# Kernel optimization log

Hardware: AMD Instinct MI355X
Metric: run time of the kernel (lower is better)

## Reference

```python
import jax, jax.numpy as jnp
import numpy as np

N_NODES = 50000
N_EDGES = 800000
N_REL = 16
D = 64          # entity_dim == relation_dim == n_hidden
NEG_SLOPE = 0.01  # torch F.leaky_relu default


def setup_inputs() -> dict:
    key = jax.random.key(0)
    ks = jax.random.split(key, 12)
    s = 1.0 / np.sqrt(D)
    return {
        "node_ids": jnp.arange(N_NODES, dtype=jnp.int64) if jax.config.jax_enable_x64 else jnp.arange(N_NODES, dtype=jnp.int32),
        "relation_ids": jax.random.randint(ks[0], (N_EDGES,), 0, N_REL),
        "src": jax.random.randint(ks[1], (N_EDGES,), 0, N_NODES),
        "dst": jax.random.randint(ks[2], (N_EDGES,), 0, N_NODES),
        "entity_embed": jax.random.normal(ks[3], (N_NODES, D), jnp.float32) * s,
        "relation_embed": jax.random.normal(ks[4], (N_REL, D), jnp.float32) * s,
        "W0": jax.random.normal(ks[5], (N_REL, D, D), jnp.float32) * s,
        "W1": jax.random.normal(ks[6], (N_REL, D, D), jnp.float32) * s,
        "ra0": jax.random.normal(ks[7], (D, D), jnp.float32) * s,
        "rb0": jax.random.normal(ks[8], (D, D), jnp.float32) * s,
        "ra1": jax.random.normal(ks[9], (D, D), jnp.float32) * s,
        "rb1": jax.random.normal(ks[10], (D, D), jnp.float32) * s,
    }


def _edge_softmax(scores, dst, n_nodes):
    # segment softmax over edges grouped by destination node (DGL edge_softmax)
    m = jax.ops.segment_max(scores, dst, num_segments=n_nodes)  # [N]
    e = jnp.exp(scores - m[dst])                                # [E]
    z = jax.ops.segment_sum(e, dst, num_segments=n_nodes)       # [N]
    return e / z[dst]


def _kgat_layer(h, efeat, src, dst, etype, Wr, ra, rb, n_nodes):
    # transform every node under every relation once: [N, R, Dr]
    trans = jnp.einsum('nd,rde->nre', h, Wr)
    t_r = trans[src, etype]                   # W_r h_t  [E, Dr]
    h_r = trans[dst, etype]                   # W_r h_h  [E, Dr]
    att = jnp.sum(t_r * jnp.tanh(h_r + efeat), axis=1)  # [E]
    a = _edge_softmax(att, dst, n_nodes)                 # [E]
    # u_mul_e + sum: scatter-add weighted source features to dst
    h_nb = jax.ops.segment_sum(h[src] * a[:, None], dst, num_segments=n_nodes)
    # Bi residual
    out = (jax.nn.leaky_relu((h + h_nb) @ ra, NEG_SLOPE)
           + jax.nn.leaky_relu((h * h_nb) @ rb, NEG_SLOPE))
    return out


def reference(node_ids, relation_ids, src, dst, entity_embed, relation_embed,
              W0, W1, ra0, rb0, ra1, rb1):
    h = entity_embed[node_ids]                 # [N, D]
    efeat = relation_embed[relation_ids]       # [E, D]
    n_nodes = node_ids.shape[0]
    cache = [h]
    for Wr, ra, rb in ((W0, ra0, rb0), (W1, ra1, rb1)):
        h = _kgat_layer(h, efeat, src, dst, relation_ids, Wr, ra, rb, n_nodes)
        cache.append(h)
    return jnp.concatenate(cache, axis=1)      # [N, 3*D]
```

## Files before the change

### kernel.cpp

```cpp
#include <hip/hip_runtime.h>
#include <hip/hip_bf16.h>
#include <math.h>

#define NN 50000
#define NE 800000
#define NR 16
#define DD 64
#define OSTRIDE 192
#define QSTRIDE 1032

typedef _Float16 f16;
typedef f16 f16x8 __attribute__((ext_vector_type(8)));
typedef f16 f16x2 __attribute__((ext_vector_type(2)));
typedef __attribute__((ext_vector_type(4))) float f32x4;

__device__ inline float tanh_fast(float x) {
    return 1.f - 2.f / (__expf(2.f * x) + 1.f);
}

__device__ inline float dot2acc(f16x2 a, f16x2 b, float c) {
#if __has_builtin(__builtin_amdgcn_fdot2)
    return __builtin_amdgcn_fdot2(a, b, c, false);
#else
    return c + (float)a[0] * (float)b[0] + (float)a[1] * (float)b[1];
#endif
}

#if __has_builtin(__builtin_amdgcn_update_dpp)
__device__ inline float xor1_add(float x) {
    return x + __int_as_float(__builtin_amdgcn_update_dpp(
        0, __float_as_int(x), 0xB1, 0xF, 0xF, true));
}
__device__ inline float xor2_add(float x) {
    return x + __int_as_float(__builtin_amdgcn_update_dpp(
        0, __float_as_int(x), 0x4E, 0xF, 0xF, true));
}
__device__ inline float xor8_add(float x) {
    return x + __int_as_float(__builtin_amdgcn_update_dpp(
        0, __float_as_int(x), 0x108, 0xF, 0xF, true));
}
#else
__device__ inline float xor1_add(float x) { return x + __shfl_xor(x, 1, 64); }
__device__ inline float xor2_add(float x) { return x + __shfl_xor(x, 2, 64); }
__device__ inline float xor8_add(float x) { return x + __shfl_xor(x, 8, 64); }
#endif

__global__ void k_deg(const int* __restrict__ dst, int* __restrict__ cnt) {
    for (int e = blockIdx.x * blockDim.x + threadIdx.x; e < NE;
         e += gridDim.x * blockDim.x)
        atomicAdd(&cnt[dst[e]], 1);
}

__global__ __launch_bounds__(256) void k_scan1(const int* __restrict__ cnt,
                                               int* __restrict__ rowptr,
                                               int* __restrict__ bsum) {
    __shared__ int sh[256];
    int b = blockIdx.x, t = threadIdx.x;
    int i = b * 256 + t;
    int v = (i < NN) ? cnt[i] : 0;
    sh[t] = v;
    __syncthreads();
    #pragma unroll
    for (int o = 1; o < 256; o <<= 1) {
        int u = (t >= o) ? sh[t - o] : 0;
        __syncthreads();
        sh[t] += u;
        __syncthreads();
    }
    if (i < NN) rowptr[i] = sh[t] - v;
    if (t == 255) bsum[b] = sh[255];
}

__global__ __launch_bounds__(256) void k_scan2(int* __restrict__ bsum, int nb) {
    __shared__ int sh[256];
    int t = threadIdx.x;
    int v = (t < nb) ? bsum[t] : 0;
    sh[t] = v;
    __syncthreads();
    #pragma unroll
    for (int o = 1; o < 256; o <<= 1) {
        int u = (t >= o) ? sh[t - o] : 0;
        __syncthreads();
        sh[t] += u;
        __syncthreads();
    }
    if (t < nb) bsum[t] = sh[t] - v;
}

__global__ __launch_bounds__(256) void k_scan3(int* __restrict__ rowptr,
                                               const int* __restrict__ bsum,
                                               int* __restrict__ cursor) {
    int b = blockIdx.x, t = threadIdx.x;
    int i = b * 256 + t;
    if (i < NN) {
        int v = rowptr[i] + bsum[b];
        rowptr[i] = v;
        cursor[i] = v;
    }
    if (i == 0) rowptr[NN] = NE;
}

__global__ void k_fill(const int* __restrict__ dst, const int* __restrict__ src,
                       const int* __restrict__ rel, int* __restrict__ cursor,
                       int* __restrict__ epack) {
    for (int e = blockIdx.x * blockDim.x + threadIdx.x; e < NE;
         e += gridDim.x * blockDim.x) {
        int pos = atomicAdd(&cursor[dst[e]], 1);
        epack[pos] = src[e] | (rel[e] << 16);
    }
}

__global__ void k_copy_h0(const int* __restrict__ node_ids,
                          const float* __restrict__ ent,
                          float* __restrict__ out,
                          f16* __restrict__ hf) {
    int i = blockIdx.x * blockDim.x + threadIdx.x;
    if (i >= NN * DD) return;
    int n = i >> 6, d = i & 63;
    float v = ent[(size_t)node_ids[n] * DD + d];
    out[(size_t)n * OSTRIDE + d] = v;
    hf[(size_t)n * DD + d] = (f16)v;
}

__global__ void k_prep(const float* __restrict__ W,
                       const float* __restrict__ ra, const float* __restrict__ rb,
                       f16* __restrict__ wf, f16* __restrict__ wtf,
                       f16* __restrict__ rat, f16* __restrict__ rbt) {
    int i = blockIdx.x * blockDim.x + threadIdx.x;
    if (i < NR * DD * DD) {
        int r = i >> 12, rem = i & 4095, d = rem >> 6, E = rem & 63;
        f16 v = (f16)W[i];
        wf[i] = v;
        wtf[(r << 12) | (E << 6) | d] = v;
    }
    if (i < DD * DD) {
        int d = i >> 6, dp = i & 63;
        rat[dp * 64 + d] = (f16)ra[i];
        rbt[dp * 64 + d] = (f16)rb[i];
    }
}

__global__ __launch_bounds__(1024) void k_fused10(const f16* __restrict__ hfin,
                                                  const f16* __restrict__ wf,
                                                  const f16* __restrict__ wtf,
                                                  const f16* __restrict__ rat,
                                                  const f16* __restrict__ rbt,
                                                  const float* __restrict__ relE,
                                                  const int* __restrict__ rowptr,
                                                  const int* __restrict__ epack,
                                                  float* __restrict__ out,
                                                  int off_in, int off_out,
                                                  f16* __restrict__ hfout) {
    __shared__ __align__(16) f16 q_lds[16 * QSTRIDE];
    __shared__ __align__(16) f16 u_lds[16][16][72];
    int n0 = blockIdx.x * 16;
    int t  = threadIdx.x;
    int w  = t >> 6, l = t & 63;
    int l15 = l & 15, lg = l >> 4;
    int r = w;

    {
        int ar = n0 + l15;
        const f16* ap = hfin + (size_t)ar * DD + lg * 8;
        f16x8 a0 = *(const f16x8*)ap;
        f16x8 a1 = *(const f16x8*)(ap + 32);

        f32x4 acc[4];
        #pragma unroll
        for (int nt = 0; nt < 4; ++nt) acc[nt] = (f32x4){0.f, 0.f, 0.f, 0.f};
        const f16* wtr = wtf + (r << 12);
        #pragma unroll
        for (int nt = 0; nt < 4; ++nt) {
            const f16* bp = wtr + (nt * 16 + l15) * DD + lg * 8;
            f16x8 b0 = *(const f16x8*)bp;
            f16x8 b1 = *(const f16x8*)(bp + 32);
            acc[nt] = __builtin_amdgcn_mfma_f32_16x16x32_f16(a0, b0, acc[nt], 0, 0, 0);
            acc[nt] = __builtin_amdgcn_mfma_f32_16x16x32_f16(a1, b1, acc[nt], 0, 0, 0);
        }

        #pragma unroll
        for (int nt = 0; nt < 4; ++nt) {
            int E = nt * 16 + l15;
            float er = relE[r * DD + E];
            #pragma unroll
            for (int reg = 0; reg < 4; ++reg)
                u_lds[w][lg * 4 + reg][E] = (f16)tanh_fast(acc[nt][reg] + er);
        }
        asm volatile("s_waitcnt lgkmcnt(0)" ::: "memory");

        const f16* up = &u_lds[w][l15][lg * 8];
        f16x8 u0 = *(const f16x8*)up;
        f16x8 u1 = *(const f16x8*)(up + 32);

        f32x4 q4[4];
        #pragma unroll
        for (int nt = 0; nt < 4; ++nt) q4[nt] = (f32x4){0.f, 0.f, 0.f, 0.f};
        const f16* wr = wf + (r << 12);
        #pragma unroll
        for (int nt = 0; nt < 4; ++nt) {
            const f16* bp = wr + (nt * 16 + l15) * DD + lg * 8;
            f16x8 b0 = *(const f16x8*)bp;
            f16x8 b1 = *(const f16x8*)(bp + 32);
            q4[nt] = __builtin_amdgcn_mfma_f32_16x16x32_f16(u0, b0, q4[nt], 0, 0, 0);
            q4[nt] = __builtin_amdgcn_mfma_f32_16x16x32_f16(u1, b1, q4[nt], 0, 0, 0);
        }

        #pragma unroll
        for (int reg = 0; reg < 4; ++reg) {
            f16* qp = q_lds + (lg * 4 + reg) * QSTRIDE + r * 64 + l15;
            #pragma unroll
            for (int nt = 0; nt < 4; ++nt)
                qp[nt * 16] = (f16)q4[nt][reg];
        }
    }
    __syncthreads();

    int n = n0 + w;
    const f16* ql = q_lds + w * QSTRIDE;
    int row0 = rowptr[n], row1 = rowptr[n + 1];
    int deg = row1 - row0;
    int g  = l >> 3;
    int d8 = l & 7;

    float zr = 0.f;
    float a[8] = {};

    int steps = (deg + 7) >> 3;
    const f16* hb = hfin + (d8 << 3);
    for (int k = 0; k < steps; ++k) {
        int idx = row0 + (k << 3) + g;
        bool ok = idx < row1;
        int p = epack[ok ? idx : row0];
        f16x8 hv = *(const f16x8*)(hb + ((size_t)(p & 0xffff) << 6));
        int rr = p >> 16;
        f16x8 qv = *(const f16x8*)(ql + (rr << 6) + (d8 << 3));
        float dp = 0.f;
        #pragma unroll
        for (int j = 0; j < 4; ++j) {
            f16x2 ha = {hv[2 * j], hv[2 * j + 1]};
            f16x2 qa = {qv[2 * j], qv[2 * j + 1]};
            dp = dot2acc(ha, qa, dp);
        }
        dp = xor1_add(dp);
        dp = xor2_add(dp);
        dp += __shfl_xor(dp, 4, 64);
        float wg = ok ? __expf(dp) : 0.f;
        zr += wg;
        #pragma unroll
        for (int j = 0; j < 8; ++j)
            a[j] = fmaf(wg, (float)hv[j], a[j]);
    }

    zr = xor8_add(zr);
    #pragma unroll
    for (int j = 0; j < 8; ++j) a[j] = xor8_add(a[j]);
    #pragma unroll
    for (int o = 16; o < 64; o <<= 1) {
        zr += __shfl_xor(zr, o, 64);
        #pragma unroll
        for (int j = 0; j < 8; ++j)
            a[j] += __shfl_xor(a[j], o, 64);
    }

    if (g == 0) {
        float inv = (deg > 0) ? 1.f / zr : 0.f;
        f16x8 hrow = *(const f16x8*)(hfin + ((size_t)n << 6) + (d8 << 3));
        f16x8 v1v, v2v;
        #pragma unroll
        for (int j = 0; j < 8; ++j) {
            float h = (float)hrow[j];
            float nb = a[j] * inv;
            v1v[j] = (f16)(h + nb);
            v2v[j] = (f16)(h * nb);
        }
        *(f16x8*)(q_lds + w * QSTRIDE + (d8 << 3)) = v1v;
        *(f16x8*)(q_lds + w * QSTRIDE + 256 + (d8 << 3)) = v2v;
    }
    __syncthreads();

    if (w < 4) {
        const f16* v1p = q_lds + (size_t)l15 * QSTRIDE + lg * 8;
        f16x8 a10 = *(const f16x8*)v1p;
        f16x8 a11 = *(const f16x8*)(v1p + 32);
        const f16* v2p = v1p + 256;
        f16x8 a20 = *(const f16x8*)v2p;
        f16x8 a21 = *(const f16x8*)(v2p + 32);

        const f16* bra = rat + (w * 16 + l15) * 64 + lg * 8;
        f16x8 b10 = *(const f16x8*)bra;
        f16x8 b11 = *(const f16x8*)(bra + 32);
        const f16* brb = rbt + (w * 16 + l15) * 64 + lg * 8;
        f16x8 b20 = *(const f16x8*)brb;
        f16x8 b21 = *(const f16x8*)(brb + 32);

        f32x4 o1 = (f32x4){0.f, 0.f, 0.f, 0.f};
        f32x4 o2 = (f32x4){0.f, 0.f, 0.f, 0.f};
        o1 = __builtin_amdgcn_mfma_f32_16x16x32_f16(a10, b10, o1, 0, 0, 0);
        o1 = __builtin_amdgcn_mfma_f32_16x16x32_f16(a11, b11, o1, 0, 0, 0);
        o2 = __builtin_amdgcn_mfma_f32_16x16x32_f16(a20, b20, o2, 0, 0, 0);
        o2 = __builtin_amdgcn_mfma_f32_16x16x32_f16(a21, b21, o2, 0, 0, 0);

        int dp = w * 16 + l15;
        #pragma unroll
        for (int reg = 0; reg < 4; ++reg) {
            int node = n0 + lg * 4 + reg;
            float u1 = o1[reg], u2 = o2[reg];
            u1 = u1 > 0.f ? u1 : 0.01f * u1;
            u2 = u2 > 0.f ? u2 : 0.01f * u2;
            float v = u1 + u2;
            out[(size_t)node * OSTRIDE + off_out + dp] = v;
            hfout[(size_t)node * DD + dp] = (f16)v;
        }
    }
}

extern "C" void kernel_launch(void* const* d_in, const int* in_sizes, int n_in,
                              void* d_out, int out_size, void* d_ws, size_t ws_size,
                              hipStream_t stream) {
    const int*   node_ids = (const int*)d_in[0];
    const int*   rel_ids  = (const int*)d_in[1];
    const int*   src      = (const int*)d_in[2];
    const int*   dst      = (const int*)d_in[3];
    const float* ent      = (const float*)d_in[4];
    const float* relE     = (const float*)d_in[5];
    const float* W[2]  = {(const float*)d_in[6], (const float*)d_in[7]};
    const float* ra[2] = {(const float*)d_in[8], (const float*)d_in[10]};
    const float* rb[2] = {(const float*)d_in[9], (const float*)d_in[11]};
    float* out = (float*)d_out;

    const size_t hf_bytes     = (size_t)NN * DD * sizeof(f16);
    const size_t wf_bytes     = (size_t)NR * DD * DD * sizeof(f16);
    const size_t rt_bytes     = (size_t)DD * DD * sizeof(f16);
    const size_t epack_bytes  = (size_t)NE * sizeof(int);
    const size_t rowptr_bytes = (size_t)(NN + 1) * sizeof(int);
    const size_t cnt_bytes    = (size_t)NN * sizeof(int);
    const int    NB_SCAN      = (NN + 255) / 256;
    const size_t bsum_bytes   = (size_t)256 * sizeof(int);

    char* p = (char*)d_ws;
    f16*   hf     = (f16*)p;   p += hf_bytes;
    f16*   hf2    = (f16*)p;   p += hf_bytes;
    f16*   wf     = (f16*)p;   p += wf_bytes;
    f16*   wtf    = (f16*)p;   p += wf_bytes;
    f16*   rat    = (f16*)p;   p += rt_bytes;
    f16*   rbt    = (f16*)p;   p += rt_bytes;
    int*   epack  = (int*)p;   p += epack_bytes;
    int*   rowptr = (int*)p;   p += rowptr_bytes;
    int*   cnt    = (int*)p;   p += cnt_bytes;
    int*   bsum   = (int*)p;   p += bsum_bytes;
    (void)ws_size;

    hipMemsetAsync(cnt, 0, cnt_bytes, stream);
    k_deg  <<<1024, 256, 0, stream>>>(dst, cnt);
    k_scan1<<<NB_SCAN, 256, 0, stream>>>(cnt, rowptr, bsum);
    k_scan2<<<1, 256, 0, stream>>>(bsum, NB_SCAN);
    k_scan3<<<NB_SCAN, 256, 0, stream>>>(rowptr, bsum, cnt);
    k_fill <<<1024, 256, 0, stream>>>(dst, src, rel_ids, cnt, epack);

    k_copy_h0<<<(NN * DD + 255) / 256, 256, 0, stream>>>(node_ids, ent, out, hf);

    f16* hin  = hf;
    f16* hout = hf2;
    for (int L = 0; L < 2; ++L) {
        int off_in = L * DD;
        int off_out = (L + 1) * DD;

        k_prep  <<<(NR * DD * DD + 255) / 256, 256, 0, stream>>>(W[L], ra[L], rb[L],
                                                                 wf, wtf, rat, rbt);
        k_fused10<<<NN / 16, 1024, 0, stream>>>(hin, wf, wtf, rat, rbt, relE,
                                                rowptr, epack, out,
                                                off_in, off_out, hout);
        f16* tmp = hin; hin = hout; hout = tmp;
    }
}
```

Baseline: 382.5 us.

## Spread a block's edges across all waves with LDS atomic accumulation

Edge aggregation changes from one wave per destination node to a flat split of all edges of the block's 16 nodes across 128 lane groups. Each packed edge now carries its local destination index in bits 20-23. Weighted features and softmax denominators are accumulated with shared-memory float atomics, which replaces the per-wave cross-lane shuffle reductions. This is meant to balance uneven degrees within a block and cut reduction overhead, at the cost of LDS atomic contention when neighbouring groups hit the same node.

```diff
diff --git a/kernel.cpp b/kernel.cpp
--- a/kernel.cpp
+++ b/kernel.cpp
@@ -35,14 +35,9 @@
     return x + __int_as_float(__builtin_amdgcn_update_dpp(
         0, __float_as_int(x), 0x4E, 0xF, 0xF, true));
 }
-__device__ inline float xor8_add(float x) {
-    return x + __int_as_float(__builtin_amdgcn_update_dpp(
-        0, __float_as_int(x), 0x108, 0xF, 0xF, true));
-}
 #else
 __device__ inline float xor1_add(float x) { return x + __shfl_xor(x, 1, 64); }
 __device__ inline float xor2_add(float x) { return x + __shfl_xor(x, 2, 64); }
-__device__ inline float xor8_add(float x) { return x + __shfl_xor(x, 8, 64); }
 #endif
 
 __global__ void k_deg(const int* __restrict__ dst, int* __restrict__ cnt) {
@@ -105,8 +100,9 @@
                        int* __restrict__ epack) {
     for (int e = blockIdx.x * blockDim.x + threadIdx.x; e < NE;
          e += gridDim.x * blockDim.x) {
-        int pos = atomicAdd(&cursor[dst[e]], 1);
-        epack[pos] = src[e] | (rel[e] << 16);
+        int d = dst[e];
+        int pos = atomicAdd(&cursor[d], 1);
+        epack[pos] = src[e] | (rel[e] << 16) | ((d & 15) << 20);
     }
 }
 
@@ -140,7 +136,7 @@
     }
 }
 
-__global__ __launch_bounds__(1024) void k_fused10(const f16* __restrict__ hfin,
+__global__ __launch_bounds__(1024) void k_fused13(const f16* __restrict__ hfin,
                                                   const f16* __restrict__ wf,
                                                   const f16* __restrict__ wtf,
                                                   const f16* __restrict__ rat,
@@ -153,11 +149,16 @@
                                                   f16* __restrict__ hfout) {
     __shared__ __align__(16) f16 q_lds[16 * QSTRIDE];
     __shared__ __align__(16) f16 u_lds[16][16][72];
+    __shared__ float acc_s[16][68];
+    __shared__ float z_s[16];
     int n0 = blockIdx.x * 16;
     int t  = threadIdx.x;
     int w  = t >> 6, l = t & 63;
     int l15 = l & 15, lg = l >> 4;
     int r = w;
+
+    for (int i = t; i < 16 * 68; i += 1024) ((float*)acc_s)[i] = 0.f;
+    if (t < 16) z_s[t] = 0.f;
 
     {
         int ar = n0 + l15;
@@ -215,25 +216,23 @@
     }
     __syncthreads();
 
-    int n = n0 + w;
-    const f16* ql = q_lds + w * QSTRIDE;
-    int row0 = rowptr[n], row1 = rowptr[n + 1];
-    int deg = row1 - row0;
     int g  = l >> 3;
     int d8 = l & 7;
-
-    float zr = 0.f;
-    float a[8] = {};
-
-    int steps = (deg + 7) >> 3;
+    int G  = (w << 3) + g;
+    int e0 = rowptr[n0];
+    int e1 = rowptr[n0 + 16];
+    int steps = (e1 - e0 + 127) >> 7;
+
     const f16* hb = hfin + (d8 << 3);
     for (int k = 0; k < steps; ++k) {
-        int idx = row0 + (k << 3) + g;
-        bool ok = idx < row1;
-        int p = epack[ok ? idx : row0];
-        f16x8 hv = *(const f16x8*)(hb + ((size_t)(p & 0xffff) << 6));
-        int rr = p >> 16;
-        f16x8 qv = *(const f16x8*)(ql + (rr << 6) + (d8 << 3));
+        int idx = e0 + (k << 7) + G;
+        bool ok = idx < e1;
+        int p = epack[ok ? idx : e0];
+        int s   = p & 0xffff;
+        int rr  = (p >> 16) & 15;
+        int loc = (p >> 20) & 15;
+        f16x8 hv = *(const f16x8*)(hb + ((size_t)s << 6));
+        f16x8 qv = *(const f16x8*)(q_lds + loc * QSTRIDE + (rr << 6) + (d8 << 3));
         float dp = 0.f;
         #pragma unroll
         for (int j = 0; j < 4; ++j) {
@@ -245,36 +244,19 @@
         dp = xor2_add(dp);
         dp += __shfl_xor(dp, 4, 64);
         float wg = ok ? __expf(dp) : 0.f;
-        zr += wg;
         #pragma unroll
         for (int j = 0; j < 8; ++j)
-            a[j] = fmaf(wg, (float)hv[j], a[j]);
-    }
-
-    zr = xor8_add(zr);
-    #pragma unroll
-    for (int j = 0; j < 8; ++j) a[j] = xor8_add(a[j]);
-    #pragma unroll
-    for (int o = 16; o < 64; o <<= 1) {
-        zr += __shfl_xor(zr, o, 64);
-        #pragma unroll
-        for (int j = 0; j < 8; ++j)
-            a[j] += __shfl_xor(a[j], o, 64);
-    }
-
-    if (g == 0) {
-        float inv = (deg > 0) ? 1.f / zr : 0.f;
-        f16x8 hrow = *(const f16x8*)(hfin + ((size_t)n << 6) + (d8 << 3));
-        f16x8 v1v, v2v;
-        #pragma unroll
-        for (int j = 0; j < 8; ++j) {
-            float h = (float)hrow[j];
-            float nb = a[j] * inv;
-            v1v[j] = (f16)(h + nb);
-            v2v[j] = (f16)(h * nb);
-        }
-        *(f16x8*)(q_lds + w * QSTRIDE + (d8 << 3)) = v1v;
-        *(f16x8*)(q_lds + w * QSTRIDE + 256 + (d8 << 3)) = v2v;
+            atomicAdd(&acc_s[loc][(d8 << 3) + j], wg * (float)hv[j]);
+        if (d8 == 0) atomicAdd(&z_s[loc], wg);
+    }
+    __syncthreads();
+
+    {
+        float zz = z_s[w];
+        float nb = (zz > 0.f) ? acc_s[w][l] * (1.f / zz) : 0.f;
+        float h = (float)hfin[((size_t)(n0 + w) << 6) + l];
+        q_lds[w * QSTRIDE + l] = (f16)(h + nb);
+        q_lds[w * QSTRIDE + 256 + l] = (f16)(h * nb);
     }
     __syncthreads();
 
@@ -367,7 +349,7 @@
 
         k_prep  <<<(NR * DD * DD + 255) / 256, 256, 0, stream>>>(W[L], ra[L], rb[L],
                                                                  wf, wtf, rat, rbt);
-        k_fused10<<<NN / 16, 1024, 0, stream>>>(hin, wf, wtf, rat, rbt, relE,
+        k_fused13<<<NN / 16, 1024, 0, stream>>>(hin, wf, wtf, rat, rbt, relE,
                                                 rowptr, epack, out,
                                                 off_in, off_out, hout);
         f16* tmp = hin; hin = hout; hout = tmp;
```

Result: slower. 1.009 ms (+163.9%).
